# Kernel optimization log

Measured on AMD Instinct MI355X. Metric: run time of the kernel, lower is better.

## Reference

```python
import jax, jax.numpy as jnp
import numpy as np

B, S, D, H = 4, 2048, 1024, 16
DH = D // H


def setup_inputs() -> dict:
    key = jax.random.key(0)
    k1, k2, k3, k4, k5 = jax.random.split(key, 5)
    X = jax.random.normal(k1, (B, S, D), dtype=jnp.float32)
    W1 = jax.random.normal(k2, (3 * D, D), dtype=jnp.float32) * 0.02
    b1 = jax.random.normal(k3, (3 * D,), dtype=jnp.float32) * 0.01
    W2 = jax.random.normal(k4, (D, D), dtype=jnp.float32) * 0.02
    b2 = jax.random.normal(k5, (D,), dtype=jnp.float32) * 0.01
    return {"X": X, "W1": W1, "b1": b1, "W2": W2, "b2": b2}


def reference(X, W1, b1, W2, b2):
    b, s, d = X.shape
    # fused QKV projection (nn.Linear: y = x @ W.T + b)
    Y = X @ W1.T + b1                                   # [B,S,3D]
    Q, K, V = jnp.split(Y, 3, axis=2)                   # each [B,S,D]
    # reshape(x): view (B,S,H,DH) then permute(0,2,3,1) -> [B,H,DH,S]
    q = Q.reshape(b, s, H, DH).transpose(0, 2, 3, 1)    # [B,H,DH,S]
    v = V.reshape(b, s, H, DH).transpose(0, 2, 3, 1)    # [B,H,DH,S]
    # reshape(x, k=True): permute(0,2,1,3) -> [B,H,S,DH]
    k = K.reshape(b, s, H, DH).transpose(0, 2, 1, 3)    # [B,H,S,DH]
    # w = q @ k / sqrt(q.size(-1)) ; note q.size(-1) == S in this layout
    w = jnp.einsum('bhds,bhse->bhde', q, k) / jnp.sqrt(jnp.asarray(s, X.dtype))  # [B,H,DH,DH]
    w = jax.nn.softmax(w, axis=-1)
    out = jnp.einsum('bhde,bhes->bhds', w, v)           # [B,H,DH,S]
    # cat(): raw contiguous view of [B,H,DH,S] into [B,S,H*DH] (memory-order reshape)
    out = out.reshape(b, s, H * DH)                     # [B,S,D]
    return out @ W2.T + b2
```

## Files before the change

kernel.cpp:

```cpp
#include <hip/hip_runtime.h>
#include <stdint.h>

#define B_ 4
#define S_ 2048
#define D_ 1024
#define H_ 16
#define DH_ 64
#define M_TOT (B_*S_)
#define N1_ (3*D_)
#define K_ D_
#define NCH 8

typedef __bf16 bf16_8 __attribute__((ext_vector_type(8)));
typedef float  f32x4  __attribute__((ext_vector_type(4)));
typedef unsigned short u16;

typedef __attribute__((address_space(1))) const void* gas_t;
typedef __attribute__((address_space(3))) void*       las_t;

__device__ __forceinline__ unsigned short f2bf(float f) {
    union { float f; unsigned u; } v; v.f = f;
    unsigned r = v.u + 0x7FFFu + ((v.u >> 16) & 1u);
    return (unsigned short)(r >> 16);
}

__device__ __forceinline__ void async_ld16(const void* g, void* l) {
    __builtin_amdgcn_global_load_lds((gas_t)g, (las_t)l, 16, 0, 0);
}

__global__ __launch_bounds__(256)
void cast_kernel(const float* __restrict__ X, const float* __restrict__ W1,
                 const float* __restrict__ W2, unsigned short* __restrict__ Xb,
                 unsigned short* __restrict__ W1b, unsigned short* __restrict__ W2b) {
    const int nX  = (M_TOT * K_) / 4;
    const int nW1 = (N1_ * K_) / 4;
    int i = blockIdx.x * 256 + threadIdx.x;
    const float4* src; unsigned short* dst; int j;
    if (i < nX)            { src = (const float4*)X;  dst = Xb;  j = i; }
    else if (i < nX + nW1) { src = (const float4*)W1; dst = W1b; j = i - nX; }
    else                   { src = (const float4*)W2; dst = W2b; j = i - nX - nW1; }
    float4 v = src[j];
    ushort4 o;
    o.x = f2bf(v.x); o.y = f2bf(v.y); o.z = f2bf(v.z); o.w = f2bf(v.w);
    ((ushort4*)dst)[j] = o;
}


#define LDA_H(AS, MH, AF) do {                                                     \
  _Pragma("unroll") for (int m_ = 0; m_ < 4; m_++)                                 \
  _Pragma("unroll") for (int ks_ = 0; ks_ < 2; ks_++) {                            \
    const int rho_ = (MH)*128 + wr*64 + m_*16 + lrow;                              \
    AF[m_][ks_] = *(const bf16_8*)((const u16*)(AS) + rho_*64 +                    \
                                   (((ks_*4+lq) ^ (lrow&7)) << 3)); } } while (0)

#define LDB_H(BS, NH, BF) do {                                                     \
  _Pragma("unroll") for (int n_ = 0; n_ < 2; n_++)                                 \
  _Pragma("unroll") for (int ks_ = 0; ks_ < 2; ks_++) {                            \
    const int rho_ = (NH)*128 + wc*32 + n_*16 + lrow;                              \
    BF[n_][ks_] = *(const bf16_8*)((const u16*)(BS) + rho_*64 +                    \
                                   (((ks_*4+lq) ^ (lrow&7)) << 3)); } } while (0)

#define MMA_Q(MH, NH, AF, BF) do {                                                 \
    __builtin_amdgcn_s_setprio(1);                                                 \
    _Pragma("unroll") for (int ks_ = 0; ks_ < 2; ks_++)                            \
    _Pragma("unroll") for (int m_ = 0; m_ < 4; m_++)                               \
    _Pragma("unroll") for (int n_ = 0; n_ < 2; n_++)                               \
        acc[(MH)*4+m_][(NH)*2+n_] = __builtin_amdgcn_mfma_f32_16x16x32_bf16(       \
            AF[m_][ks_], BF[n_][ks_], acc[(MH)*4+m_][(NH)*2+n_], 0, 0, 0);         \
    __builtin_amdgcn_s_setprio(0);                                                 \
  } while (0)

#define BAR()      __builtin_amdgcn_s_barrier()
#define WAIT_LGKM() asm volatile("s_waitcnt lgkmcnt(0)" ::: "memory")

template<int N, int NBX, int KK, bool OUT_BF16>
__global__ __launch_bounds__(512, 2)
void gemm_bt2(const u16* __restrict__ A, const u16* __restrict__ Bm,
              const float* __restrict__ bias, void* __restrict__ C) {
    __shared__ u16 As[2][256 * 64];
    __shared__ u16 Bs[2][256 * 64];

    const int t    = threadIdx.x;
    const int wid  = t >> 6;
    const int lane = t & 63;
    const int lrow = lane & 15;
    const int lq   = lane >> 4;
    const int wr   = wid >> 2;
    const int wc   = wid & 3;

    const int lid  = blockIdx.y * NBX + blockIdx.x;
    const int xcd  = lid & 7;
    const int slot = lid >> 3;
    const int by   = xcd * (gridDim.y >> 3) + slot / NBX;
    const int bx   = slot % NBX;
    const int m0   = by * 256;
    const int n0   = bx * 256;

    const u16* Ab = A  + (size_t)m0 * KK;
    const u16* Bb = Bm + (size_t)n0 * KK;

    f32x4 acc[8][4] = {};

    auto STG = [&](const u16* __restrict__ G, char* lds, int half, int k0, bool isA) {
#pragma unroll
        for (int cc = 0; cc < 2; cc++) {
            const int rho = half * 128 + cc * 64 + (t >> 3);
            const int blk = t & 7;
            const int g   = isA ? (((rho >> 6) & 1) * 128 + ((rho >> 7) & 1) * 64 + (rho & 63))
                                : (((rho >> 5) & 3) * 64  + ((rho >> 7) & 1) * 32 + (rho & 31));
            async_ld16(G + (size_t)g * KK + k0 + ((blk ^ (rho & 7)) << 3),
                       lds + rho * 128 + blk * 16);
        }
    };

    char* as0 = (char*)&As[0][0]; char* as1 = (char*)&As[1][0];
    char* bs0 = (char*)&Bs[0][0]; char* bs1 = (char*)&Bs[1][0];

    STG(Ab, as0, 0, 0,  true);
    STG(Bb, bs0, 0, 0,  false);
    STG(Bb, bs0, 1, 0,  false);
    STG(Ab, as0, 1, 0,  true);
    STG(Ab, as1, 0, 64, true);
    STG(Bb, bs1, 0, 64, false);
    STG(Bb, bs1, 1, 64, false);
    asm volatile("s_waitcnt vmcnt(6)" ::: "memory");
    BAR();

    bf16_8 af[4][2], blo[2][2], bhi[2][2];

    constexpr int NT = KK / 64;
    constexpr int NI = NT / 2;

    for (int i = 0; i < NI; ++i) {
        const bool pf = (i < NI - 1);
        const int kE = (2 * i + 2) * 64;
        const int kO = (2 * i + 3) * 64;

        LDA_H(as0, 0, af);
        LDB_H(bs0, 0, blo);
        STG(Ab, as1, 1, (2 * i + 1) * 64, true);
        BAR(); WAIT_LGKM();
        MMA_Q(0, 0, af, blo);
        BAR();
        LDB_H(bs0, 1, bhi);
        if (pf) STG(Ab, as0, 0, kE, true);
        BAR(); WAIT_LGKM();
        MMA_Q(0, 1, af, bhi);
        BAR();
        LDA_H(as0, 1, af);
        if (pf) STG(Bb, bs0, 0, kE, false);
        BAR(); WAIT_LGKM();
        MMA_Q(1, 1, af, bhi);
        BAR();
        if (pf) STG(Bb, bs0, 1, kE, false);
        BAR();
        MMA_Q(1, 0, af, blo);
        if (pf) { asm volatile("s_waitcnt vmcnt(6)" ::: "memory"); }
        else    { asm volatile("s_waitcnt vmcnt(0)" ::: "memory"); }
        BAR();
        LDA_H(as1, 0, af);
        LDB_H(bs1, 0, blo);
        if (pf) STG(Ab, as0, 1, kE, true);
        BAR(); WAIT_LGKM();
        MMA_Q(0, 0, af, blo);
        BAR();
        LDB_H(bs1, 1, bhi);
        if (pf) STG(Ab, as1, 0, kO, true);
        BAR(); WAIT_LGKM();
        MMA_Q(0, 1, af, bhi);
        BAR();
        LDA_H(as1, 1, af);
        if (pf) STG(Bb, bs1, 0, kO, false);
        BAR(); WAIT_LGKM();
        MMA_Q(1, 1, af, bhi);
        BAR();
        if (pf) STG(Bb, bs1, 1, kO, false);
        BAR();
        MMA_Q(1, 0, af, blo);
        if (pf) asm volatile("s_waitcnt vmcnt(6)" ::: "memory");
        BAR();
    }

#pragma unroll
    for (int nt = 0; nt < 4; nt++) {
        const int col = n0 + wc * 64 + nt * 16 + lrow;
        const float bv = bias[col];
#pragma unroll
        for (int mt = 0; mt < 8; mt++) {
            const int row = m0 + wr * 128 + mt * 16 + lq * 4;
            f32x4 a = acc[mt][nt];
            if (OUT_BF16) {
                u16* Cp = (u16*)C;
#pragma unroll
                for (int i2 = 0; i2 < 4; i2++)
                    Cp[(size_t)(row + i2) * N + col] = f2bf(a[i2] + bv);
            } else {
                float* Cp = (float*)C;
#pragma unroll
                for (int i2 = 0; i2 < 4; i2++)
                    Cp[(size_t)(row + i2) * N + col] = a[i2] + bv;
            }
        }
    }
}

__global__ __launch_bounds__(256)
void attn_scores(const unsigned short* __restrict__ Y, float* __restrict__ Scp) {
    __shared__ unsigned short Qs[64 * 72];
    __shared__ unsigned short Ks[64 * 72];
    const int bh = blockIdx.x, ch = blockIdx.y;
    const int b = bh >> 4, h = bh & 15;
    const size_t ybase = (size_t)b * S_ * 3072;
    const int qoff = h * 64, koff = D_ + h * 64;
    const int t = threadIdx.x, wid = t >> 6, lane = t & 63;
    const int lrow = lane & 15, lq = lane >> 4;

    f32x4 acc[4] = {};
    const int sbeg = ch * (S_ / NCH);
    for (int s0 = sbeg; s0 < sbeg + S_ / NCH; s0 += 64) {
#pragma unroll
        for (int p = 0; p < 4; p++) {
            int idx = p * 256 + t;
            int r = idx >> 4, cg = (idx & 15) * 4;
            const size_t gb = ybase + (size_t)(s0 + r) * 3072;
            ushort4 q4 = *(const ushort4*)(Y + gb + qoff + cg);
            ushort4 k4 = *(const ushort4*)(Y + gb + koff + cg);
            Qs[(cg + 0) * 72 + r] = q4.x; Qs[(cg + 1) * 72 + r] = q4.y;
            Qs[(cg + 2) * 72 + r] = q4.z; Qs[(cg + 3) * 72 + r] = q4.w;
            Ks[(cg + 0) * 72 + r] = k4.x; Ks[(cg + 1) * 72 + r] = k4.y;
            Ks[(cg + 2) * 72 + r] = k4.z; Ks[(cg + 3) * 72 + r] = k4.w;
        }
        __syncthreads();
#pragma unroll
        for (int ks = 0; ks < 2; ks++) {
            bf16_8 aq = *(const bf16_8*)(Qs + (wid * 16 + lrow) * 72 + ks * 32 + lq * 8);
#pragma unroll
            for (int nt = 0; nt < 4; nt++) {
                bf16_8 bk = *(const bf16_8*)(Ks + (nt * 16 + lrow) * 72 + ks * 32 + lq * 8);
                acc[nt] = __builtin_amdgcn_mfma_f32_16x16x32_bf16(aq, bk, acc[nt], 0, 0, 0);
            }
        }
        __syncthreads();
    }

    float* out = Scp + (size_t)(bh * NCH + ch) * 64 * 64;
#pragma unroll
    for (int nt = 0; nt < 4; nt++)
#pragma unroll
        for (int i = 0; i < 4; i++)
            out[(wid * 16 + lq * 4 + i) * 64 + nt * 16 + lrow] = acc[nt][i];
}

__global__ __launch_bounds__(256)
void attn_softmax(const float* __restrict__ Scp, unsigned short* __restrict__ Wb) {
    const int bh = blockIdx.x;
    const int t = threadIdx.x;
    const int d = t >> 2, q = t & 3;
    float s[16] = {};
#pragma unroll
    for (int c = 0; c < NCH; c++) {
        const float4* p = (const float4*)(Scp + ((size_t)(bh * NCH + c) * 64 + d) * 64 + q * 16);
#pragma unroll
        for (int j = 0; j < 4; j++) {
            float4 v = p[j];
            s[j*4+0] += v.x; s[j*4+1] += v.y; s[j*4+2] += v.z; s[j*4+3] += v.w;
        }
    }
    const float scale = 0.022097086912079608f;
    float m = -3.0e38f;
#pragma unroll
    for (int i = 0; i < 16; i++) { s[i] *= scale; m = fmaxf(m, s[i]); }
    m = fmaxf(m, __shfl_xor(m, 1));
    m = fmaxf(m, __shfl_xor(m, 2));
    float sum = 0.f;
#pragma unroll
    for (int i = 0; i < 16; i++) { s[i] = __expf(s[i] - m); sum += s[i]; }
    sum += __shfl_xor(sum, 1);
    sum += __shfl_xor(sum, 2);
    const float inv = 1.0f / sum;
    unsigned short* w = Wb + (size_t)bh * 4096 + d * 64 + q * 16;
    ushort4 o0, o1, o2, o3;
    o0.x=f2bf(s[0]*inv);  o0.y=f2bf(s[1]*inv);  o0.z=f2bf(s[2]*inv);  o0.w=f2bf(s[3]*inv);
    o1.x=f2bf(s[4]*inv);  o1.y=f2bf(s[5]*inv);  o1.z=f2bf(s[6]*inv);  o1.w=f2bf(s[7]*inv);
    o2.x=f2bf(s[8]*inv);  o2.y=f2bf(s[9]*inv);  o2.z=f2bf(s[10]*inv); o2.w=f2bf(s[11]*inv);
    o3.x=f2bf(s[12]*inv); o3.y=f2bf(s[13]*inv); o3.z=f2bf(s[14]*inv); o3.w=f2bf(s[15]*inv);
    ((ushort4*)w)[0]=o0; ((ushort4*)w)[1]=o1; ((ushort4*)w)[2]=o2; ((ushort4*)w)[3]=o3;
}

__global__ __launch_bounds__(256)
void attn_out(const unsigned short* __restrict__ Y, const unsigned short* __restrict__ Wb,
              unsigned short* __restrict__ O) {
    __shared__ unsigned short Ws[64 * 72];
    const int bh = blockIdx.x, sc = blockIdx.y;
    const int b = bh >> 4, h = bh & 15;
    const size_t ybase = (size_t)b * S_ * 3072;
    const int voff = 2 * D_ + h * 64;
    const int t = threadIdx.x, wid = t >> 6, lane = t & 63;
    const int lrow = lane & 15, lq = lane >> 4;

    {
        const int d = t >> 2, q = t & 3;
        const uint4* src = (const uint4*)(Wb + (size_t)bh * 4096 + d * 64 + q * 16);
        uint4* dst = (uint4*)(Ws + d * 72 + q * 16);
        dst[0] = src[0];
        *(uint4*)(Ws + d * 72 + q * 16 + 8) = src[1];
    }
    __syncthreads();

    bf16_8 aw[4][2];
#pragma unroll
    for (int mt = 0; mt < 4; mt++)
#pragma unroll
        for (int ks = 0; ks < 2; ks++)
            aw[mt][ks] = *(const bf16_8*)(Ws + (mt * 16 + lrow) * 72 + ks * 32 + lq * 8);

    const size_t obase = (size_t)b * (H_ * DH_ * S_) + (size_t)h * (DH_ * S_);
    const int s0 = sc * 256 + wid * 64;
    f32x4 o[4][4] = {};
#pragma unroll
    for (int ks = 0; ks < 2; ks++) {
        bf16_8 bv[4];
#pragma unroll
        for (int nt = 0; nt < 4; nt++)
            bv[nt] = *(const bf16_8*)(Y + ybase + (size_t)(s0 + nt * 16 + lrow) * 3072 + voff + ks * 32 + lq * 8);
#pragma unroll
        for (int mt = 0; mt < 4; mt++)
#pragma unroll
            for (int nt = 0; nt < 4; nt++)
                o[mt][nt] = __builtin_amdgcn_mfma_f32_16x16x32_bf16(aw[mt][ks], bv[nt], o[mt][nt], 0, 0, 0);
    }
#pragma unroll
    for (int mt = 0; mt < 4; mt++)
#pragma unroll
        for (int nt = 0; nt < 4; nt++) {
            const int d = mt * 16 + lq * 4;
            const int s = s0 + nt * 16 + lrow;
#pragma unroll
            for (int i = 0; i < 4; i++)
                O[obase + (size_t)(d + i) * S_ + s] = f2bf(o[mt][nt][i]);
        }
}

extern "C" void kernel_launch(void* const* d_in, const int* in_sizes, int n_in,
                              void* d_out, int out_size, void* d_ws, size_t ws_size,
                              hipStream_t stream) {
    const float* X  = (const float*)d_in[0];
    const float* W1 = (const float*)d_in[1];
    const float* b1 = (const float*)d_in[2];
    const float* W2 = (const float*)d_in[3];
    const float* b2 = (const float*)d_in[4];

    char* ws = (char*)d_ws;
    unsigned short* Xb  = (unsigned short*)(ws + 0);
    unsigned short* W1b = (unsigned short*)(ws + (16u << 20));
    unsigned short* W2b = (unsigned short*)(ws + (22u << 20));
    unsigned short* Yb  = (unsigned short*)(ws + (24u << 20));
    unsigned short* Wb  = (unsigned short*)(ws + 0);
    unsigned short* Ob  = (unsigned short*)(ws + (1u << 20));
    float* Scp = (float*)d_out;

    cast_kernel<<<12288, 256, 0, stream>>>(X, W1, W2, Xb, W1b, W2b);
    gemm_bt2<N1_, N1_/256, K_, true ><<<dim3(N1_ / 256, M_TOT / 256), 512, 0, stream>>>(Xb, W1b, b1, Yb);
    attn_scores<<<dim3(64, NCH), 256, 0, stream>>>(Yb, Scp);
    attn_softmax<<<64, 256, 0, stream>>>(Scp, Wb);
    attn_out<<<dim3(64, NCH), 256, 0, stream>>>(Yb, Wb, Ob);
    gemm_bt2<D_, D_/256, K_, false><<<dim3(D_ / 256, M_TOT / 256), 512, 0, stream>>>(Ob, W2b, b2, d_out);
}
```

Baseline: 230.3 us.

## Use smaller-tile single-buffered GEMM for output projection and relax launch bounds

Adds a simpler 128x128-tile, 256-thread GEMM kernel and uses it for the output projection in place of the 256x256 double-buffered kernel, which gives that GEMM four times as many blocks (512 instead of 128) across the device. The large kernel's launch bounds drop from 2 to 1 blocks per CU, and its LDS wait now carries a sched_barrier to stop the compiler moving instructions across it. In exchange, the new kernel has no double buffering and syncs twice per K step, and the larger kernel may lose occupancy.

Result: faster. 221.9 us (-3.6%).

```diff
diff --git a/kernel.cpp b/kernel.cpp
--- a/kernel.cpp
+++ b/kernel.cpp
@@ -45,6 +45,91 @@
     ((ushort4*)dst)[j] = o;
 }
 
+template<int N, int NBX, bool OUT_BF16>
+__global__ __launch_bounds__(256)
+void gemm_bt(const unsigned short* __restrict__ A,
+             const unsigned short* __restrict__ Bm,
+             const float* __restrict__ bias,
+             void* __restrict__ C, int K) {
+    __shared__ unsigned short As[128 * 64];
+    __shared__ unsigned short Bs[128 * 64];
+    const int t    = threadIdx.x;
+    const int wid  = t >> 6;
+    const int lane = t & 63;
+    const int lrow = lane & 15;
+    const int lq   = lane >> 4;
+
+    const int lid  = blockIdx.y * NBX + blockIdx.x;
+    const int xcd  = lid & 7;
+    const int slot = lid >> 3;
+    const int by   = xcd * (gridDim.y >> 3) + slot / NBX;
+    const int bx   = slot % NBX;
+    const int m0   = by * 128;
+    const int n0   = bx * 128;
+
+    const int wm   = (wid >> 1) * 64;
+    const int wn   = (wid & 1) * 64;
+
+    f32x4 acc[4][4] = {};
+
+    for (int k0 = 0; k0 < K; k0 += 64) {
+#pragma unroll
+        for (int p = 0; p < 4; p++) {
+            const int c   = p * 256 + t;
+            const int row = c >> 3;
+            const int kb  = (c & 7) ^ (row & 7);
+            async_ld16(A  + (size_t)(m0 + row) * K + k0 + kb * 8, (char*)As + c * 16);
+            async_ld16(Bm + (size_t)(n0 + row) * K + k0 + kb * 8, (char*)Bs + c * 16);
+        }
+        __syncthreads();
+
+#pragma unroll
+        for (int ks = 0; ks < 2; ks++) {
+            bf16_8 af[4], bfr[4];
+#pragma unroll
+            for (int mt = 0; mt < 4; mt++) {
+                const int r  = wm + mt * 16 + lrow;
+                const int kb = (ks * 4 + lq) ^ (r & 7);
+                af[mt] = *(const bf16_8*)(As + (r * 8 + kb) * 8);
+            }
+#pragma unroll
+            for (int nt = 0; nt < 4; nt++) {
+                const int r  = wn + nt * 16 + lrow;
+                const int kb = (ks * 4 + lq) ^ (r & 7);
+                bfr[nt] = *(const bf16_8*)(Bs + (r * 8 + kb) * 8);
+            }
+#pragma unroll
+            for (int mt = 0; mt < 4; mt++)
+#pragma unroll
+                for (int nt = 0; nt < 4; nt++)
+                    acc[mt][nt] = __builtin_amdgcn_mfma_f32_16x16x32_bf16(af[mt], bfr[nt], acc[mt][nt], 0, 0, 0);
+        }
+        __syncthreads();
+    }
+
+#pragma unroll
+    for (int nt = 0; nt < 4; nt++) {
+        const int col = n0 + wn + nt * 16 + lrow;
+        const float bv = bias[col];
+#pragma unroll
+        for (int mt = 0; mt < 4; mt++) {
+            const int row = m0 + wm + mt * 16 + lq * 4;
+            f32x4 a = acc[mt][nt];
+            if (OUT_BF16) {
+                unsigned short* Cp = (unsigned short*)C;
+#pragma unroll
+                for (int i = 0; i < 4; i++)
+                    Cp[(size_t)(row + i) * N + col] = f2bf(a[i] + bv);
+            } else {
+                float* Cp = (float*)C;
+#pragma unroll
+                for (int i = 0; i < 4; i++)
+                    Cp[(size_t)(row + i) * N + col] = a[i] + bv;
+            }
+        }
+    }
+}
+
 
 #define LDA_H(AS, MH, AF) do {                                                     \
   _Pragma("unroll") for (int m_ = 0; m_ < 4; m_++)                                 \
@@ -70,11 +155,12 @@
     __builtin_amdgcn_s_setprio(0);                                                 \
   } while (0)
 
-#define BAR()      __builtin_amdgcn_s_barrier()
-#define WAIT_LGKM() asm volatile("s_waitcnt lgkmcnt(0)" ::: "memory")
+#define BAR()       __builtin_amdgcn_s_barrier()
+#define WAIT_LGKM() do { asm volatile("s_waitcnt lgkmcnt(0)" ::: "memory");        \
+                         __builtin_amdgcn_sched_barrier(0); } while (0)
 
 template<int N, int NBX, int KK, bool OUT_BF16>
-__global__ __launch_bounds__(512, 2)
+__global__ __launch_bounds__(512, 1)
 void gemm_bt2(const u16* __restrict__ A, const u16* __restrict__ Bm,
               const float* __restrict__ bias, void* __restrict__ C) {
     __shared__ u16 As[2][256 * 64];
@@ -360,9 +446,9 @@
     float* Scp = (float*)d_out;
 
     cast_kernel<<<12288, 256, 0, stream>>>(X, W1, W2, Xb, W1b, W2b);
-    gemm_bt2<N1_, N1_/256, K_, true ><<<dim3(N1_ / 256, M_TOT / 256), 512, 0, stream>>>(Xb, W1b, b1, Yb);
+    gemm_bt2<N1_, N1_/256, K_, true><<<dim3(N1_ / 256, M_TOT / 256), 512, 0, stream>>>(Xb, W1b, b1, Yb);
     attn_scores<<<dim3(64, NCH), 256, 0, stream>>>(Yb, Scp);
     attn_softmax<<<64, 256, 0, stream>>>(Scp, Wb);
     attn_out<<<dim3(64, NCH), 256, 0, stream>>>(Yb, Wb, Ob);
-    gemm_bt2<D_, D_/256, K_, false><<<dim3(D_ / 256, M_TOT / 256), 512, 0, stream>>>(Ob, W2b, b2, d_out);
-}
+    gemm_bt<D_, D_/128, false><<<dim3(D_ / 128, M_TOT / 128), 256, 0, stream>>>(Ob, W2b, b2, d_out, K_);
+}
```
